# Kernel optimization log

Measured on AMD Instinct MI355X. Metric: run time of the kernel, lower is better.

## Reference

```python
import jax, jax.numpy as jnp
import numpy as np

NEG = jnp.float32(-1e30)  # finite stand-in for -inf (grad-safe)
BLANK = 0


def setup_inputs() -> dict:
    key = jax.random.key(0)
    k1, k2, k3, k4 = jax.random.split(key, 4)
    B, T, V, S = 64, 1024, 128, 256
    logits = jax.random.normal(k1, (B, T, V), dtype=jnp.float32)
    log_probs = jax.nn.log_softmax(logits, axis=-1)  # valid log-probs like a model head
    log_probs_length = jax.random.randint(k2, (B,), 768, T + 1)
    text_encoded = jax.random.randint(k3, (B, S), 1, V)  # labels exclude blank=0
    text_encoded_length = jax.random.randint(k4, (B,), 64, S + 1)
    return {
        "log_probs": log_probs,
        "log_probs_length": log_probs_length,
        "text_encoded": text_encoded,
        "text_encoded_length": text_encoded_length,
    }


def _ctc_loss(log_probs, input_lengths, targets, target_lengths):
    """CTC loss, matching torch.nn.CTCLoss(blank=0, reduction='mean', zero_infinity=True)."""
    B, T, V = log_probs.shape
    S = targets.shape[1]
    L2 = 2 * S + 1  # extended label sequence: blank-interleaved

    # extended labels ext[b, s]: blank at even s, target[(s-1)//2] at odd s
    ext = jnp.full((B, L2), BLANK, dtype=targets.dtype)
    ext = ext.at[:, 1::2].set(targets)

    # gather per-step log-prob of each extended label: [B, T, L2]
    lp_ext = jnp.take_along_axis(
        log_probs, jnp.broadcast_to(ext[:, None, :], (B, T, L2)), axis=2
    )

    pos = jnp.arange(L2)
    valid_s = pos[None, :] < (2 * target_lengths[:, None] + 1)  # [B, L2]
    ext_m2 = jnp.pad(ext, ((0, 0), (2, 0)), constant_values=BLANK)[:, :-2]
    # skip transition s-2 -> s allowed only at non-blank (odd) positions with differing labels
    skip_mask = (pos[None, :] >= 2) & (pos[None, :] % 2 == 1) & (ext != ext_m2)

    alpha0 = jnp.full((B, L2), NEG, dtype=log_probs.dtype)
    alpha0 = alpha0.at[:, 0].set(lp_ext[:, 0, 0])
    alpha0 = alpha0.at[:, 1].set(jnp.where(target_lengths > 0, lp_ext[:, 0, 1], NEG))
    alpha0 = jnp.where(valid_s, alpha0, NEG)

    lp_ext_T = jnp.moveaxis(lp_ext, 1, 0)  # [T, B, L2]

    def step(alpha, x):
        lp_t, t = x
        s1 = jnp.pad(alpha, ((0, 0), (1, 0)), constant_values=NEG)[:, :-1]
        s2 = jnp.pad(alpha, ((0, 0), (2, 0)), constant_values=NEG)[:, :-2]
        a = jnp.logaddexp(alpha, s1)
        a = jnp.where(skip_mask, jnp.logaddexp(a, s2), a)
        new = jnp.where(valid_s, a + lp_t, NEG)
        # freeze alpha for samples whose input sequence has ended
        new = jnp.where((t < input_lengths)[:, None], new, alpha)
        return new, None

    alpha, _ = jax.lax.scan(step, alpha0, (lp_ext_T[1:], jnp.arange(1, T)))

    L = target_lengths
    idx1 = (2 * L)[:, None]
    idx0 = jnp.maximum(2 * L - 1, 0)[:, None]
    a_blank = jnp.take_along_axis(alpha, idx1, axis=1)[:, 0]
    a_label = jnp.take_along_axis(alpha, idx0, axis=1)[:, 0]
    ll = jnp.logaddexp(a_blank, jnp.where(L > 0, a_label, NEG))
    loss_b = -ll
    # zero_infinity: zero out infeasible alignments
    loss_b = jnp.where(loss_b > 1e29, jnp.float32(0.0), loss_b)
    # reduction='mean': divide each loss by its target length, then batch-mean
    return jnp.mean(loss_b / jnp.maximum(L, 1).astype(log_probs.dtype))


def reference(log_probs, log_probs_length, text_encoded, text_encoded_length):
    return _ctc_loss(log_probs, log_probs_length, text_encoded, text_encoded_length)
```

## Files before the change

### kernel.cpp

```cpp
#include <hip/hip_runtime.h>

constexpr int B_ = 64;
constexpr int T_ = 1024;
constexpr int V_ = 128;
constexpr int S_ = 256;
constexpr int GRING = 32;
constexpr int ROWF = 384;
constexpr int NGW = 5;
constexpr float INV_LN2 = 1.4426950408889634f;
constexpr float LN2 = 0.6931471805599453f;

#define WG_SCOPE __HIP_MEMORY_SCOPE_WORKGROUP

template<int CTRL>
__device__ __forceinline__ float dppf(float x) {
    return __int_as_float(__builtin_amdgcn_update_dpp(
        0, __float_as_int(x), CTRL, 0xF, 0xF, false));
}
constexpr int DPP_WAVE_SHR1 = 0x138;
constexpr int DPP_WAVE_SHL1 = 0x130;
constexpr int DPP_ROW_SHR1  = 0x111;
constexpr int DPP_ROW_SHR2  = 0x112;
constexpr int DPP_ROW_SHR4  = 0x114;
constexpr int DPP_ROW_SHR8  = 0x118;
constexpr int DPP_BCAST15   = 0x142;
constexpr int DPP_BCAST31   = 0x143;

__device__ __forceinline__ void poll_eq(int* p, int want) {
    while (__hip_atomic_load(p, __ATOMIC_RELAXED, WG_SCOPE) != want)
        __builtin_amdgcn_s_sleep(1);
}

__device__ __forceinline__ int wave_rescale(float a[10], int& K) {
    float mx = a[0];
    #pragma unroll
    for (int k = 1; k < 10; ++k) mx = fmaxf(mx, a[k]);
    mx = fmaxf(mx, dppf<DPP_ROW_SHR1>(mx));
    mx = fmaxf(mx, dppf<DPP_ROW_SHR2>(mx));
    mx = fmaxf(mx, dppf<DPP_ROW_SHR4>(mx));
    mx = fmaxf(mx, dppf<DPP_ROW_SHR8>(mx));
    mx = fmaxf(mx, dppf<DPP_BCAST15>(mx));
    mx = fmaxf(mx, dppf<DPP_BCAST31>(mx));
    const unsigned mb = (unsigned)__builtin_amdgcn_readlane(__float_as_uint(mx), 63);
    const int ks = (mb != 0u) ? (250 - (int)(mb >> 23)) : 0;
    #pragma unroll
    for (int k = 0; k < 10; ++k) a[k] = ldexpf(a[k], ks);
    K += ks;
    return ks;
}

__global__ __launch_bounds__(768) void ctc_fused7(
    const float* __restrict__ lp,
    const int* __restrict__ in_len,
    const int* __restrict__ tgt,
    const int* __restrict__ tgt_len,
    float* __restrict__ ws)
{
    const int b    = blockIdx.x;
    const int tid  = threadIdx.x;
    const int wid  = tid >> 6;
    const int lane = tid & 63;

    __shared__ float ringF[GRING * ROWF];
    __shared__ float ringB[GRING * ROWF];
    __shared__ float dumpA[640];
    __shared__ float dumpB[640];
    __shared__ int   tagF[8], tagB[8];
    __shared__ int   consF, consB;
    __shared__ int   KFsh, KBsh;

    const int L  = tgt_len[b];
    const int Tb = in_len[b];
    const float* lpb = lp + (size_t)b * T_ * V_;
    const int* tg = tgt + b * S_;

    const int tm = (Tb - 2) >> 1;
    const int Uf = tm;
    const int Ub = Tb - 2 - tm;

    if (tid == 0) { consF = 0; consB = 0; }
    if (tid < 8) tagF[tid] = -1;
    else if (tid < 16) tagB[tid - 8] = -1;
    __syncthreads();

    if (wid >= 2) {
        const int dir = (wid - 2) / NGW;
        const int q   = (wid - 2) % NGW;
        const int U   = dir ? Ub : Uf;
        float* ring   = dir ? ringB : ringF;
        int*   tags   = dir ? tagB  : tagF;
        int*   consp  = dir ? &consB : &consF;

        int   labE[5];
        float vmask[5];
        #pragma unroll
        for (int c = 0; c < 5; ++c) {
            const int j = 5 * lane + c;
            if (j < L) { labE[c] = tg[j]; vmask[c] = 1.0f; }
            else       { labE[c] = 0;     vmask[c] = 0.0f; }
        }

        for (int m = q; 4 * m + 1 <= U; m += NGW) {
            const int n = min(4, U - 4 * m);
            float v[4][6];
            #pragma unroll
            for (int r = 0; r < 4; ++r) {
                if (r < n) {
                    const int u = 4 * m + 1 + r;
                    const int t = dir ? (Tb - 1 - u) : u;
                    const float* row = lpb + (size_t)t * V_;
                    v[r][0] = row[0];
                    #pragma unroll
                    for (int c = 0; c < 5; ++c) v[r][c + 1] = row[labE[c]];
                }
            }
            while (__hip_atomic_load(consp, __ATOMIC_RELAXED, WG_SCOPE) < 4 * m - 28)
                __builtin_amdgcn_s_sleep(1);
            #pragma unroll
            for (int r = 0; r < 4; ++r) {
                if (r < n) {
                    const int u = 4 * m + 1 + r;
                    float e[6];
                    e[0] = __builtin_exp2f(v[r][0] * INV_LN2);
                    #pragma unroll
                    for (int c = 0; c < 5; ++c)
                        e[c + 1] = vmask[c] * __builtin_exp2f(v[r][c + 1] * INV_LN2);
                    float* rb = ring + ((u - 1) & (GRING - 1)) * ROWF;
                    ((float2*)rb)[lane]         = make_float2(e[0], e[1]);
                    ((float2*)(rb + 128))[lane] = make_float2(e[2], e[3]);
                    ((float2*)(rb + 256))[lane] = make_float2(e[4], e[5]);
                }
            }
            if (lane == 0)
                __hip_atomic_store(&tags[m & 7], m, __ATOMIC_RELEASE, WG_SCOPE);
        }
    } else if (wid == 0) {
        float skipf[5];
        #pragma unroll
        for (int c = 0; c < 5; ++c) {
            const int j = 5 * lane + c;
            skipf[c] = (j >= 1 && j < L && tg[j] != tg[j - 1]) ? 1.0f : 0.0f;
        }
        float a[10];
        #pragma unroll
        for (int k = 0; k < 10; ++k) a[k] = 0.0f;
        {
            const float p00 = __builtin_exp2f(lpb[0] * INV_LN2);
            const float p01 = __builtin_exp2f(lpb[tg[0]] * INV_LN2);
            if (lane == 0) { a[0] = p00; a[1] = p01; }
        }
        float u9n = 0.0f;
        int K = 0;

        float2 S[4][12];
        auto readBlock = [&](int set, int m) {
            const int base = ((4 * m) & (GRING - 1)) * ROWF + 2 * lane;
            #pragma unroll
            for (int r = 0; r < 4; ++r)
                #pragma unroll
                for (int pl = 0; pl < 3; ++pl)
                    S[set][r * 3 + pl] =
                        *(const float2*)&ringF[base + r * ROWF + pl * 128];
        };
        auto rowCore = [&](float2 c0, float2 c1, float2 c2) {
            const float u9 = u9n;
            const float p0 = c0.x;
            a[9] = (a[9] + a[8] + skipf[4] * a[7]) * c2.y;
            u9n = dppf<DPP_WAVE_SHR1>(a[9]);
            a[8] = (a[8] + a[7]) * p0;
            a[7] = (a[7] + a[6] + skipf[3] * a[5]) * c2.x;
            a[6] = (a[6] + a[5]) * p0;
            a[5] = (a[5] + a[4] + skipf[2] * a[3]) * c1.y;
            a[4] = (a[4] + a[3]) * p0;
            a[3] = (a[3] + a[2] + skipf[1] * a[1]) * c1.x;
            a[2] = (a[2] + a[1]) * p0;
            a[1] = (a[1] + a[0] + skipf[0] * u9) * c0.y;
            a[0] = (a[0] + u9) * p0;
        };
        auto row4 = [&](int set) {
            #pragma unroll
            for (int r = 0; r < 4; ++r)
                rowCore(S[set][r * 3], S[set][r * 3 + 1], S[set][r * 3 + 2]);
        };
        auto body = [&](int m, int setc, int setp) {
            if (4 * (m + 2) + 1 <= Uf) {
                poll_eq(&tagF[(m + 2) & 7], m + 2);
                readBlock(setp, m + 2);
            }
            row4(setc);
            if (lane == 0)
                __hip_atomic_store(&consF, 4 * m + 4, __ATOMIC_RELAXED, WG_SCOPE);
        };

        const int MB4 = (Uf / 4) & ~3;
        poll_eq(&tagF[0], 0); readBlock(0, 0);
        poll_eq(&tagF[1], 1); readBlock(1, 1);
        for (int mb = 0; mb < MB4; mb += 4) {
            body(mb + 0, 0, 2);
            body(mb + 1, 1, 3);
            { const int ks = wave_rescale(a, K); u9n = ldexpf(u9n, ks); }
            body(mb + 2, 2, 0);
            body(mb + 3, 3, 1);
            { const int ks = wave_rescale(a, K); u9n = ldexpf(u9n, ks); }
        }
        #pragma unroll
        for (int r = 0; r < 4; ++r)
            if (4 * MB4 + 1 + r <= Uf)
                rowCore(S[0][r * 3], S[0][r * 3 + 1], S[0][r * 3 + 2]);
        #pragma unroll
        for (int r = 0; r < 4; ++r)
            if (4 * MB4 + 5 + r <= Uf)
                rowCore(S[1][r * 3], S[1][r * 3 + 1], S[1][r * 3 + 2]);
        { const int ks = wave_rescale(a, K); u9n = ldexpf(u9n, ks); }
        for (int u = 4 * MB4 + 9; u <= Uf; ++u) {
            const int bu = (u - 1) >> 2;
            poll_eq(&tagF[bu & 7], bu);
            const int base = ((u - 1) & (GRING - 1)) * ROWF + 2 * lane;
            const float2 c0 = *(const float2*)&ringF[base];
            const float2 c1 = *(const float2*)&ringF[base + 128];
            const float2 c2 = *(const float2*)&ringF[base + 256];
            rowCore(c0, c1, c2);
        }

        #pragma unroll
        for (int k = 0; k < 10; ++k) dumpA[10 * lane + k] = a[k];
        if (lane == 0) {
            KFsh = K;
            __hip_atomic_store(&consF, Uf + 64, __ATOMIC_RELAXED, WG_SCOPE);
        }
    } else {
        float sB[5];
        #pragma unroll
        for (int c = 0; c < 5; ++c) {
            const int j = 5 * lane + c + 1;
            sB[c] = (j < L && tg[j] != tg[j - 1]) ? 1.0f : 0.0f;
        }
        float g[10];
        #pragma unroll
        for (int k = 0; k < 10; ++k) g[k] = 0.0f;
        {
            const float pb = __builtin_exp2f(lpb[(size_t)(Tb - 1) * V_] * INV_LN2);
            const float pl = __builtin_exp2f(lpb[(size_t)(Tb - 1) * V_ + tg[L - 1]] * INV_LN2);
            #pragma unroll
            for (int k = 0; k < 10; ++k) {
                const int s = 10 * lane + k;
                if (s == 2 * L)     g[k] = pb;
                if (s == 2 * L - 1) g[k] = pl;
            }
        }
        float d0n = dppf<DPP_WAVE_SHL1>(g[0]);
        float d1n = dppf<DPP_WAVE_SHL1>(g[1]);
        int K = 0;

        float2 S[4][12];
        auto readBlock = [&](int set, int m) {
            const int base = ((4 * m) & (GRING - 1)) * ROWF + 2 * lane;
            #pragma unroll
            for (int r = 0; r < 4; ++r)
                #pragma unroll
                for (int pl = 0; pl < 3; ++pl)
                    S[set][r * 3 + pl] =
                        *(const float2*)&ringB[base + r * ROWF + pl * 128];
        };
        auto rowCore = [&](float2 c0, float2 c1, float2 c2) {
            const float d0 = d0n, d1 = d1n;
            const float p0 = c0.x;
            g[0] = (g[0] + g[1]) * p0;
            g[1] = (g[1] + g[2] + sB[0] * g[3]) * c0.y;
            d0n = dppf<DPP_WAVE_SHL1>(g[0]);
            d1n = dppf<DPP_WAVE_SHL1>(g[1]);
            g[2] = (g[2] + g[3]) * p0;
            g[3] = (g[3] + g[4] + sB[1] * g[5]) * c1.x;
            g[4] = (g[4] + g[5]) * p0;
            g[5] = (g[5] + g[6] + sB[2] * g[7]) * c1.y;
            g[6] = (g[6] + g[7]) * p0;
            g[7] = (g[7] + g[8] + sB[3] * g[9]) * c2.x;
            g[8] = (g[8] + g[9]) * p0;
            g[9] = (g[9] + d0 + sB[4] * d1) * c2.y;
        };
        auto row4 = [&](int set) {
            #pragma unroll
            for (int r = 0; r < 4; ++r)
                rowCore(S[set][r * 3], S[set][r * 3 + 1], S[set][r * 3 + 2]);
        };
        auto body = [&](int m, int setc, int setp) {
            if (4 * (m + 2) + 1 <= Ub) {
                poll_eq(&tagB[(m + 2) & 7], m + 2);
                readBlock(setp, m + 2);
            }
            row4(setc);
            if (lane == 0)
                __hip_atomic_store(&consB, 4 * m + 4, __ATOMIC_RELAXED, WG_SCOPE);
        };

        const int MB4 = (Ub / 4) & ~3;
        poll_eq(&tagB[0], 0); readBlock(0, 0);
        poll_eq(&tagB[1], 1); readBlock(1, 1);
        for (int mb = 0; mb < MB4; mb += 4) {
            body(mb + 0, 0, 2);
            body(mb + 1, 1, 3);
            { const int ks = wave_rescale(g, K);
              d0n = ldexpf(d0n, ks); d1n = ldexpf(d1n, ks); }
            body(mb + 2, 2, 0);
            body(mb + 3, 3, 1);
            { const int ks = wave_rescale(g, K);
              d0n = ldexpf(d0n, ks); d1n = ldexpf(d1n, ks); }
        }
        #pragma unroll
        for (int r = 0; r < 4; ++r)
            if (4 * MB4 + 1 + r <= Ub)
                rowCore(S[0][r * 3], S[0][r * 3 + 1], S[0][r * 3 + 2]);
        #pragma unroll
        for (int r = 0; r < 4; ++r)
            if (4 * MB4 + 5 + r <= Ub)
                rowCore(S[1][r * 3], S[1][r * 3 + 1], S[1][r * 3 + 2]);
        { const int ks = wave_rescale(g, K);
          d0n = ldexpf(d0n, ks); d1n = ldexpf(d1n, ks); }
        for (int u = 4 * MB4 + 9; u <= Ub; ++u) {
            const int bu = (u - 1) >> 2;
            poll_eq(&tagB[bu & 7], bu);
            const int base = ((u - 1) & (GRING - 1)) * ROWF + 2 * lane;
            const float2 c0 = *(const float2*)&ringB[base];
            const float2 c1 = *(const float2*)&ringB[base + 128];
            const float2 c2 = *(const float2*)&ringB[base + 256];
            rowCore(c0, c1, c2);
        }

        {
            const float d0 = d0n, d1 = d1n;
            g[0] = g[0] + g[1];
            g[1] = g[1] + g[2] + sB[0] * g[3];
            g[2] = g[2] + g[3];
            g[3] = g[3] + g[4] + sB[1] * g[5];
            g[4] = g[4] + g[5];
            g[5] = g[5] + g[6] + sB[2] * g[7];
            g[6] = g[6] + g[7];
            g[7] = g[7] + g[8] + sB[3] * g[9];
            g[8] = g[8] + g[9];
            g[9] = g[9] + d0 + sB[4] * d1;
        }
        #pragma unroll
        for (int k = 0; k < 10; ++k) dumpB[10 * lane + k] = g[k];
        if (lane == 0) {
            KBsh = K;
            __hip_atomic_store(&consB, Ub + 64, __ATOMIC_RELAXED, WG_SCOPE);
        }
    }

    __syncthreads();
    if (wid == 0) {
        double sum = 0.0;
        #pragma unroll
        for (int k = 0; k < 10; ++k)
            sum += (double)dumpA[10 * lane + k] * (double)dumpB[10 * lane + k];
        #pragma unroll
        for (int d = 1; d < 64; d <<= 1) sum += __shfl_xor(sum, d, 64);
        if (lane == 0) {
            float loss = 0.0f;
            if (sum > 0.0) {
                const long long ub = __double_as_longlong(sum);
                const int ex = (int)((ub >> 52) & 2047) - 1023;
                const double f = __longlong_as_double(
                    (ub & 0x000FFFFFFFFFFFFFLL) | 0x3FF0000000000000LL);
                const float ll2 = __builtin_log2f((float)f)
                                + (float)(ex - KFsh - KBsh);
                loss = -(ll2 * LN2);
                if (!(loss <= 1e29f)) loss = 0.0f;
            }
            ws[b] = loss / (float)L;
        }
    }
}

__global__ void ctc_reduce_kernel(const float* __restrict__ ws, float* __restrict__ out) {
    float v = ws[threadIdx.x];
    #pragma unroll
    for (int o = 32; o > 0; o >>= 1) v += __shfl_down(v, o);
    if (threadIdx.x == 0) out[0] = v / (float)B_;
}

extern "C" void kernel_launch(void* const* d_in, const int* in_sizes, int n_in,
                              void* d_out, int out_size, void* d_ws, size_t ws_size,
                              hipStream_t stream) {
    const float* lp      = (const float*)d_in[0];
    const int*   in_len  = (const int*)d_in[1];
    const int*   tgt     = (const int*)d_in[2];
    const int*   tgt_len = (const int*)d_in[3];
    float* loss = (float*)d_ws;
    float* out  = (float*)d_out;

    ctc_fused7<<<B_, 768, 0, stream>>>(lp, in_len, tgt, tgt_len, loss);
    ctc_reduce_kernel<<<1, 64, 0, stream>>>(loss, out);
}
```

Measured before the change: 137.1 us.

## Fuse final reduction into main kernel and double-buffer producer loads

Drops the separate reduce kernel: each block writes its loss plus a magic flag at agent scope, and block 0 spins on all flags before summing. The block grows to 1024 threads, but six waves return immediately so that producer waves sit at chosen slots. It also cuts producers per direction from five to four, has producers issue the next block's global loads before processing the current one, and lets the forward wave combine directly with the backward result instead of using a workgroup barrier. This aims to remove a launch and some sync cost. The risks are the cross-block spin, which relies on all blocks being resident, and a magic flag in the workspace that may persist across calls.

```diff
diff --git a/kernel.cpp b/kernel.cpp
--- a/kernel.cpp
+++ b/kernel.cpp
@@ -6,11 +6,13 @@
 constexpr int S_ = 256;
 constexpr int GRING = 32;
 constexpr int ROWF = 384;
-constexpr int NGW = 5;
+constexpr int NGW = 4;
 constexpr float INV_LN2 = 1.4426950408889634f;
 constexpr float LN2 = 0.6931471805599453f;
+constexpr unsigned MAGIC = 0x5AD0F00Du;
 
 #define WG_SCOPE __HIP_MEMORY_SCOPE_WORKGROUP
+#define AG_SCOPE __HIP_MEMORY_SCOPE_AGENT
 
 template<int CTRL>
 __device__ __forceinline__ float dppf(float x) {
@@ -28,6 +30,10 @@
 
 __device__ __forceinline__ void poll_eq(int* p, int want) {
     while (__hip_atomic_load(p, __ATOMIC_RELAXED, WG_SCOPE) != want)
+        __builtin_amdgcn_s_sleep(1);
+}
+__device__ __forceinline__ void poll_ge(int* p, int want) {
+    while (__hip_atomic_load(p, __ATOMIC_RELAXED, WG_SCOPE) < want)
         __builtin_amdgcn_s_sleep(1);
 }
 
@@ -49,12 +55,14 @@
     return ks;
 }
 
-__global__ __launch_bounds__(768) void ctc_fused7(
+__global__ __launch_bounds__(1024) void ctc_fused8(
     const float* __restrict__ lp,
     const int* __restrict__ in_len,
     const int* __restrict__ tgt,
     const int* __restrict__ tgt_len,
-    float* __restrict__ ws)
+    float* __restrict__ wloss,
+    int* __restrict__ wflag,
+    float* __restrict__ out)
 {
     const int b    = blockIdx.x;
     const int tid  = threadIdx.x;
@@ -63,11 +71,10 @@
 
     __shared__ float ringF[GRING * ROWF];
     __shared__ float ringB[GRING * ROWF];
-    __shared__ float dumpA[640];
     __shared__ float dumpB[640];
     __shared__ int   tagF[8], tagB[8];
     __shared__ int   consF, consB;
-    __shared__ int   KFsh, KBsh;
+    __shared__ int   KBsh;
 
     const int L  = tgt_len[b];
     const int Tb = in_len[b];
@@ -83,9 +90,13 @@
     else if (tid < 16) tagB[tid - 8] = -1;
     __syncthreads();
 
+    if (wid == 4 || wid == 5 || wid == 8 || wid == 9 || wid == 12 || wid == 13)
+        return;
+
     if (wid >= 2) {
-        const int dir = (wid - 2) / NGW;
-        const int q   = (wid - 2) % NGW;
+        const int gi  = (wid >> 2) * 2 + (wid & 1);
+        const int dir = (gi >= 4) ? 1 : 0;
+        const int q   = dir ? (gi - 4) : gi;
         const int U   = dir ? Ub : Uf;
         float* ring   = dir ? ringB : ringF;
         int*   tags   = dir ? tagB  : tagF;
@@ -100,9 +111,9 @@
             else       { labE[c] = 0;     vmask[c] = 0.0f; }
         }
 
-        for (int m = q; 4 * m + 1 <= U; m += NGW) {
+        float vA[4][6], vB[4][6];
+        auto issueLoads = [&](float (&v)[4][6], int m) {
             const int n = min(4, U - 4 * m);
-            float v[4][6];
             #pragma unroll
             for (int r = 0; r < 4; ++r) {
                 if (r < n) {
@@ -114,6 +125,9 @@
                     for (int c = 0; c < 5; ++c) v[r][c + 1] = row[labE[c]];
                 }
             }
+        };
+        auto processBlock = [&](float (&v)[4][6], int m) {
+            const int n = min(4, U - 4 * m);
             while (__hip_atomic_load(consp, __ATOMIC_RELAXED, WG_SCOPE) < 4 * m - 28)
                 __builtin_amdgcn_s_sleep(1);
             #pragma unroll
@@ -133,102 +147,26 @@
             }
             if (lane == 0)
                 __hip_atomic_store(&tags[m & 7], m, __ATOMIC_RELEASE, WG_SCOPE);
-        }
-    } else if (wid == 0) {
-        float skipf[5];
-        #pragma unroll
-        for (int c = 0; c < 5; ++c) {
-            const int j = 5 * lane + c;
-            skipf[c] = (j >= 1 && j < L && tg[j] != tg[j - 1]) ? 1.0f : 0.0f;
-        }
-        float a[10];
-        #pragma unroll
-        for (int k = 0; k < 10; ++k) a[k] = 0.0f;
-        {
-            const float p00 = __builtin_exp2f(lpb[0] * INV_LN2);
-            const float p01 = __builtin_exp2f(lpb[tg[0]] * INV_LN2);
-            if (lane == 0) { a[0] = p00; a[1] = p01; }
-        }
-        float u9n = 0.0f;
-        int K = 0;
-
-        float2 S[4][12];
-        auto readBlock = [&](int set, int m) {
-            const int base = ((4 * m) & (GRING - 1)) * ROWF + 2 * lane;
-            #pragma unroll
-            for (int r = 0; r < 4; ++r)
-                #pragma unroll
-                for (int pl = 0; pl < 3; ++pl)
-                    S[set][r * 3 + pl] =
-                        *(const float2*)&ringF[base + r * ROWF + pl * 128];
-        };
-        auto rowCore = [&](float2 c0, float2 c1, float2 c2) {
-            const float u9 = u9n;
-            const float p0 = c0.x;
-            a[9] = (a[9] + a[8] + skipf[4] * a[7]) * c2.y;
-            u9n = dppf<DPP_WAVE_SHR1>(a[9]);
-            a[8] = (a[8] + a[7]) * p0;
-            a[7] = (a[7] + a[6] + skipf[3] * a[5]) * c2.x;
-            a[6] = (a[6] + a[5]) * p0;
-            a[5] = (a[5] + a[4] + skipf[2] * a[3]) * c1.y;
-            a[4] = (a[4] + a[3]) * p0;
-            a[3] = (a[3] + a[2] + skipf[1] * a[1]) * c1.x;
-            a[2] = (a[2] + a[1]) * p0;
-            a[1] = (a[1] + a[0] + skipf[0] * u9) * c0.y;
-            a[0] = (a[0] + u9) * p0;
-        };
-        auto row4 = [&](int set) {
-            #pragma unroll
-            for (int r = 0; r < 4; ++r)
-                rowCore(S[set][r * 3], S[set][r * 3 + 1], S[set][r * 3 + 2]);
-        };
-        auto body = [&](int m, int setc, int setp) {
-            if (4 * (m + 2) + 1 <= Uf) {
-                poll_eq(&tagF[(m + 2) & 7], m + 2);
-                readBlock(setp, m + 2);
-            }
-            row4(setc);
-            if (lane == 0)
-                __hip_atomic_store(&consF, 4 * m + 4, __ATOMIC_RELAXED, WG_SCOPE);
-        };
-
-        const int MB4 = (Uf / 4) & ~3;
-        poll_eq(&tagF[0], 0); readBlock(0, 0);
-        poll_eq(&tagF[1], 1); readBlock(1, 1);
-        for (int mb = 0; mb < MB4; mb += 4) {
-            body(mb + 0, 0, 2);
-            body(mb + 1, 1, 3);
-            { const int ks = wave_rescale(a, K); u9n = ldexpf(u9n, ks); }
-            body(mb + 2, 2, 0);
-            body(mb + 3, 3, 1);
-            { const int ks = wave_rescale(a, K); u9n = ldexpf(u9n, ks); }
-        }
-        #pragma unroll
-        for (int r = 0; r < 4; ++r)
-            if (4 * MB4 + 1 + r <= Uf)
-                rowCore(S[0][r * 3], S[0][r * 3 + 1], S[0][r * 3 + 2]);
-        #pragma unroll
-        for (int r = 0; r < 4; ++r)
-            if (4 * MB4 + 5 + r <= Uf)
-                rowCore(S[1][r * 3], S[1][r * 3 + 1], S[1][r * 3 + 2]);
-        { const int ks = wave_rescale(a, K); u9n = ldexpf(u9n, ks); }
-        for (int u = 4 * MB4 + 9; u <= Uf; ++u) {
-            const int bu = (u - 1) >> 2;
-            poll_eq(&tagF[bu & 7], bu);
-            const int base = ((u - 1) & (GRING - 1)) * ROWF + 2 * lane;
-            const float2 c0 = *(const float2*)&ringF[base];
-            const float2 c1 = *(const float2*)&ringF[base + 128];
-            const float2 c2 = *(const float2*)&ringF[base + 256];
-            rowCore(c0, c1, c2);
-        }
-
-        #pragma unroll
-        for (int k = 0; k < 10; ++k) dumpA[10 * lane + k] = a[k];
-        if (lane == 0) {
-            KFsh = K;
-            __hip_atomic_store(&consF, Uf + 64, __ATOMIC_RELAXED, WG_SCOPE);
-        }
-    } else {
+        };
+
+        int mA = q;
+        bool haveA = (4 * mA + 1 <= U);
+        if (haveA) issueLoads(vA, mA);
+        while (haveA) {
+            const int mB = mA + NGW;
+            const bool haveB = (4 * mB + 1 <= U);
+            if (haveB) issueLoads(vB, mB);
+            processBlock(vA, mA);
+            const int mA2 = mB + NGW;
+            const bool haveA2 = (4 * mA2 + 1 <= U);
+            if (haveA2) issueLoads(vA, mA2);
+            if (haveB) processBlock(vB, mB);
+            mA = mA2; haveA = haveA2;
+        }
+        return;
+    }
+
+    if (wid == 1) {
         float sB[5];
         #pragma unroll
         for (int c = 0; c < 5; ++c) {
@@ -252,15 +190,14 @@
         float d1n = dppf<DPP_WAVE_SHL1>(g[1]);
         int K = 0;
 
-        float2 S[4][12];
-        auto readBlock = [&](int set, int m) {
+        float2 S0[12], S1[12];
+        auto readBlock = [&](float2 (&S)[12], int m) {
             const int base = ((4 * m) & (GRING - 1)) * ROWF + 2 * lane;
             #pragma unroll
             for (int r = 0; r < 4; ++r)
                 #pragma unroll
                 for (int pl = 0; pl < 3; ++pl)
-                    S[set][r * 3 + pl] =
-                        *(const float2*)&ringB[base + r * ROWF + pl * 128];
+                    S[r * 3 + pl] = *(const float2*)&ringB[base + r * ROWF + pl * 128];
         };
         auto rowCore = [&](float2 c0, float2 c1, float2 c2) {
             const float d0 = d0n, d1 = d1n;
@@ -278,52 +215,36 @@
             g[8] = (g[8] + g[9]) * p0;
             g[9] = (g[9] + d0 + sB[4] * d1) * c2.y;
         };
-        auto row4 = [&](int set) {
-            #pragma unroll
-            for (int r = 0; r < 4; ++r)
-                rowCore(S[set][r * 3], S[set][r * 3 + 1], S[set][r * 3 + 2]);
-        };
-        auto body = [&](int m, int setc, int setp) {
-            if (4 * (m + 2) + 1 <= Ub) {
-                poll_eq(&tagB[(m + 2) & 7], m + 2);
-                readBlock(setp, m + 2);
-            }
-            row4(setc);
-            if (lane == 0)
-                __hip_atomic_store(&consB, 4 * m + 4, __ATOMIC_RELAXED, WG_SCOPE);
-        };
-
-        const int MB4 = (Ub / 4) & ~3;
-        poll_eq(&tagB[0], 0); readBlock(0, 0);
-        poll_eq(&tagB[1], 1); readBlock(1, 1);
-        for (int mb = 0; mb < MB4; mb += 4) {
-            body(mb + 0, 0, 2);
-            body(mb + 1, 1, 3);
+        auto row4 = [&](float2 (&S)[12]) {
+            #pragma unroll
+            for (int r = 0; r < 4; ++r) rowCore(S[r * 3], S[r * 3 + 1], S[r * 3 + 2]);
+        };
+
+        const int FB = Ub >> 2;
+        poll_eq(&tagB[0], 0); readBlock(S0, 0);
+        int mb = 0;
+        for (; mb + 2 <= FB; mb += 2) {
+            if (mb + 1 < FB) { poll_eq(&tagB[(mb + 1) & 7], mb + 1); readBlock(S1, mb + 1); }
+            row4(S0);
+            if (lane == 0) __hip_atomic_store(&consB, 4 * mb + 4, __ATOMIC_RELAXED, WG_SCOPE);
+            if (mb + 2 < FB) { poll_eq(&tagB[(mb + 2) & 7], mb + 2); readBlock(S0, mb + 2); }
+            row4(S1);
+            if (lane == 0) __hip_atomic_store(&consB, 4 * mb + 8, __ATOMIC_RELAXED, WG_SCOPE);
             { const int ks = wave_rescale(g, K);
               d0n = ldexpf(d0n, ks); d1n = ldexpf(d1n, ks); }
-            body(mb + 2, 2, 0);
-            body(mb + 3, 3, 1);
+        }
+        if (mb < FB) {
+            row4(S0);
+            if (lane == 0) __hip_atomic_store(&consB, 4 * mb + 4, __ATOMIC_RELAXED, WG_SCOPE);
             { const int ks = wave_rescale(g, K);
               d0n = ldexpf(d0n, ks); d1n = ldexpf(d1n, ks); }
         }
-        #pragma unroll
-        for (int r = 0; r < 4; ++r)
-            if (4 * MB4 + 1 + r <= Ub)
-                rowCore(S[0][r * 3], S[0][r * 3 + 1], S[0][r * 3 + 2]);
-        #pragma unroll
-        for (int r = 0; r < 4; ++r)
-            if (4 * MB4 + 5 + r <= Ub)
-                rowCore(S[1][r * 3], S[1][r * 3 + 1], S[1][r * 3 + 2]);
-        { const int ks = wave_rescale(g, K);
-          d0n = ldexpf(d0n, ks); d1n = ldexpf(d1n, ks); }
-        for (int u = 4 * MB4 + 9; u <= Ub; ++u) {
-            const int bu = (u - 1) >> 2;
-            poll_eq(&tagB[bu & 7], bu);
+        for (int u = 4 * FB + 1; u <= Ub; ++u) {
+            poll_eq(&tagB[FB & 7], FB);
             const int base = ((u - 1) & (GRING - 1)) * ROWF + 2 * lane;
-            const float2 c0 = *(const float2*)&ringB[base];
-            const float2 c1 = *(const float2*)&ringB[base + 128];
-            const float2 c2 = *(const float2*)&ringB[base + 256];
-            rowCore(c0, c1, c2);
+            rowCore(*(const float2*)&ringB[base],
+                    *(const float2*)&ringB[base + 128],
+                    *(const float2*)&ringB[base + 256]);
         }
 
         {
@@ -345,38 +266,112 @@
             KBsh = K;
             __hip_atomic_store(&consB, Ub + 64, __ATOMIC_RELAXED, WG_SCOPE);
         }
-    }
-
-    __syncthreads();
-    if (wid == 0) {
-        double sum = 0.0;
-        #pragma unroll
-        for (int k = 0; k < 10; ++k)
-            sum += (double)dumpA[10 * lane + k] * (double)dumpB[10 * lane + k];
-        #pragma unroll
-        for (int d = 1; d < 64; d <<= 1) sum += __shfl_xor(sum, d, 64);
-        if (lane == 0) {
-            float loss = 0.0f;
-            if (sum > 0.0) {
-                const long long ub = __double_as_longlong(sum);
-                const int ex = (int)((ub >> 52) & 2047) - 1023;
-                const double f = __longlong_as_double(
-                    (ub & 0x000FFFFFFFFFFFFFLL) | 0x3FF0000000000000LL);
-                const float ll2 = __builtin_log2f((float)f)
-                                + (float)(ex - KFsh - KBsh);
-                loss = -(ll2 * LN2);
-                if (!(loss <= 1e29f)) loss = 0.0f;
-            }
-            ws[b] = loss / (float)L;
-        }
-    }
-}
-
-__global__ void ctc_reduce_kernel(const float* __restrict__ ws, float* __restrict__ out) {
-    float v = ws[threadIdx.x];
-    #pragma unroll
-    for (int o = 32; o > 0; o >>= 1) v += __shfl_down(v, o);
-    if (threadIdx.x == 0) out[0] = v / (float)B_;
+        return;
+    }
+
+    float skipf[5];
+    #pragma unroll
+    for (int c = 0; c < 5; ++c) {
+        const int j = 5 * lane + c;
+        skipf[c] = (j >= 1 && j < L && tg[j] != tg[j - 1]) ? 1.0f : 0.0f;
+    }
+    float a[10];
+    #pragma unroll
+    for (int k = 0; k < 10; ++k) a[k] = 0.0f;
+    {
+        const float p00 = __builtin_exp2f(lpb[0] * INV_LN2);
+        const float p01 = __builtin_exp2f(lpb[tg[0]] * INV_LN2);
+        if (lane == 0) { a[0] = p00; a[1] = p01; }
+    }
+    float u9n = 0.0f;
+    int K = 0;
+
+    float2 S0[12], S1[12];
+    auto readBlock = [&](float2 (&S)[12], int m) {
+        const int base = ((4 * m) & (GRING - 1)) * ROWF + 2 * lane;
+        #pragma unroll
+        for (int r = 0; r < 4; ++r)
+            #pragma unroll
+            for (int pl = 0; pl < 3; ++pl)
+                S[r * 3 + pl] = *(const float2*)&ringF[base + r * ROWF + pl * 128];
+    };
+    auto rowCore = [&](float2 c0, float2 c1, float2 c2) {
+        const float u9 = u9n;
+        const float p0 = c0.x;
+        a[9] = (a[9] + a[8] + skipf[4] * a[7]) * c2.y;
+        u9n = dppf<DPP_WAVE_SHR1>(a[9]);
+        a[8] = (a[8] + a[7]) * p0;
+        a[7] = (a[7] + a[6] + skipf[3] * a[5]) * c2.x;
+        a[6] = (a[6] + a[5]) * p0;
+        a[5] = (a[5] + a[4] + skipf[2] * a[3]) * c1.y;
+        a[4] = (a[4] + a[3]) * p0;
+        a[3] = (a[3] + a[2] + skipf[1] * a[1]) * c1.x;
+        a[2] = (a[2] + a[1]) * p0;
+        a[1] = (a[1] + a[0] + skipf[0] * u9) * c0.y;
+        a[0] = (a[0] + u9) * p0;
+    };
+    auto row4 = [&](float2 (&S)[12]) {
+        #pragma unroll
+        for (int r = 0; r < 4; ++r) rowCore(S[r * 3], S[r * 3 + 1], S[r * 3 + 2]);
+    };
+
+    const int FB = Uf >> 2;
+    poll_eq(&tagF[0], 0); readBlock(S0, 0);
+    int mb = 0;
+    for (; mb + 2 <= FB; mb += 2) {
+        if (mb + 1 < FB) { poll_eq(&tagF[(mb + 1) & 7], mb + 1); readBlock(S1, mb + 1); }
+        row4(S0);
+        if (lane == 0) __hip_atomic_store(&consF, 4 * mb + 4, __ATOMIC_RELAXED, WG_SCOPE);
+        if (mb + 2 < FB) { poll_eq(&tagF[(mb + 2) & 7], mb + 2); readBlock(S0, mb + 2); }
+        row4(S1);
+        if (lane == 0) __hip_atomic_store(&consF, 4 * mb + 8, __ATOMIC_RELAXED, WG_SCOPE);
+        { const int ks = wave_rescale(a, K); u9n = ldexpf(u9n, ks); }
+    }
+    if (mb < FB) {
+        row4(S0);
+        if (lane == 0) __hip_atomic_store(&consF, 4 * mb + 4, __ATOMIC_RELAXED, WG_SCOPE);
+        { const int ks = wave_rescale(a, K); u9n = ldexpf(u9n, ks); }
+    }
+    for (int u = 4 * FB + 1; u <= Uf; ++u) {
+        poll_eq(&tagF[FB & 7], FB);
+        const int base = ((u - 1) & (GRING - 1)) * ROWF + 2 * lane;
+        rowCore(*(const float2*)&ringF[base],
+                *(const float2*)&ringF[base + 128],
+                *(const float2*)&ringF[base + 256]);
+    }
+    if (lane == 0) __hip_atomic_store(&consF, Uf + 64, __ATOMIC_RELAXED, WG_SCOPE);
+
+    poll_ge(&consB, Ub + 64);
+    double sum = 0.0;
+    #pragma unroll
+    for (int k = 0; k < 10; ++k)
+        sum += (double)a[k] * (double)dumpB[10 * lane + k];
+    #pragma unroll
+    for (int d = 1; d < 64; d <<= 1) sum += __shfl_xor(sum, d, 64);
+
+    if (lane == 0) {
+        float loss = 0.0f;
+        if (sum > 0.0) {
+            const long long ub2 = __double_as_longlong(sum);
+            const int ex = (int)((ub2 >> 52) & 2047) - 1023;
+            const double f = __longlong_as_double(
+                (ub2 & 0x000FFFFFFFFFFFFFLL) | 0x3FF0000000000000LL);
+            const float ll2 = __builtin_log2f((float)f) + (float)(ex - K - KBsh);
+            loss = -(ll2 * LN2);
+            if (!(loss <= 1e29f)) loss = 0.0f;
+        }
+        wloss[b] = loss / (float)L;
+        __hip_atomic_store(&wflag[b], (int)MAGIC, __ATOMIC_RELEASE, AG_SCOPE);
+    }
+
+    if (b == 0) {
+        while ((unsigned)__hip_atomic_load(&wflag[lane], __ATOMIC_ACQUIRE, AG_SCOPE) != MAGIC)
+            __builtin_amdgcn_s_sleep(1);
+        float v = wloss[lane];
+        #pragma unroll
+        for (int o = 1; o < 64; o <<= 1) v += __shfl_xor(v, o, 64);
+        if (lane == 0) out[0] = v / (float)B_;
+    }
 }
 
 extern "C" void kernel_launch(void* const* d_in, const int* in_sizes, int n_in,
@@ -386,9 +381,9 @@
     const int*   in_len  = (const int*)d_in[1];
     const int*   tgt     = (const int*)d_in[2];
     const int*   tgt_len = (const int*)d_in[3];
-    float* loss = (float*)d_ws;
-    float* out  = (float*)d_out;
-
-    ctc_fused7<<<B_, 768, 0, stream>>>(lp, in_len, tgt, tgt_len, loss);
-    ctc_reduce_kernel<<<1, 64, 0, stream>>>(loss, out);
-}
+    float* wloss = (float*)d_ws;
+    int*   wflag = (int*)((char*)d_ws + 256);
+    float* out   = (float*)d_out;
+
+    ctc_fused8<<<B_, 1024, 0, stream>>>(lp, in_len, tgt, tgt_len, wloss, wflag, out);
+}
```

Result: slower. 142.9 us (+4.3%).
